# Kernel tuning notes

Hardware: AMD Instinct MI355X
Metric: run time of the kernel (lower is better)

The kernel has to match this reference:

```python
import jax, jax.numpy as jnp
import numpy as np
import math


def butterfly_mult_untied(twiddle, x, increasing_stride=True):
    """twiddle: (nstack, m, n//2, 2, 2); x: (batch, nstack, n)."""
    b, nstack, n = x.shape
    m = twiddle.shape[1]
    out = x
    for idx in range(m):  # loop over log2(n) stages (structural, not data dim)
        log_stride = idx if increasing_stride else m - 1 - idx
        stride = 1 << log_stride
        nb = n // (2 * stride)
        # (nstack, nb, stride, 2, 2) -> (nstack, nb, 2, 2, stride)
        t = jnp.transpose(twiddle[:, idx].reshape(nstack, nb, stride, 2, 2), (0, 1, 3, 4, 2))
        o = out.reshape(b, nstack, nb, 1, 2, stride)
        out = (t * o).sum(axis=4).reshape(b, nstack, n)
    return out


def setup_inputs() -> dict:
    key = jax.random.key(0)
    k1, k2, k3 = jax.random.split(key, 3)
    batch, in_size, out_size = 32768, 1024, 1024
    m = int(math.ceil(math.log2(in_size)))  # 10
    nstack = 1
    x = jax.random.normal(k1, (batch, in_size), dtype=jnp.float32)
    # 'regular' non-ortho init: randn / sqrt(2)
    twiddle = jax.random.normal(k2, (nstack, m, in_size // 2, 2, 2), dtype=jnp.float32) / math.sqrt(2)
    bound = 1 / math.sqrt(in_size)
    bias = jax.random.uniform(k3, (out_size,), dtype=jnp.float32, minval=-bound, maxval=bound)
    return {"x": x, "twiddle": twiddle, "bias": bias}


def reference(x, twiddle, bias):
    batch, in_size = x.shape
    nstack = twiddle.shape[0]
    out_size = bias.shape[0]
    # pre_process: in_size is a power of 2 and nstack==1 -> just stack
    out = jnp.broadcast_to(x[:, None, :], (batch, nstack, in_size))
    out = butterfly_mult_untied(twiddle, out, increasing_stride=True)
    # post_process: flatten nstack, slice to out_size, add bias
    out = out.reshape(batch, nstack * in_size)[:, :out_size] + bias
    return out
```

## Files before the change

kernel.cpp:

```cpp
#include <hip/hip_runtime.h>


constexpr int N = 1024;
constexpr int B_ROWS = 4;
constexpr int WAVES = 4;
constexpr int WBUF  = 1344;


template<int ST>
__device__ __forceinline__ void stageA(float (&v)[4][16],
                                       const float4* __restrict__ tw4,
                                       const int lane)
{
    constexpr int s = 1 << ST;
    #pragma unroll
    for (int pi = 0; pi < 8; ++pi) {
        const int jl = ((pi >> ST) << (ST + 1)) | (pi & (s - 1));
        const int jh = jl + s;
        const int e  = 16 * lane + jl;
        const int pr = ((e >> (ST + 1)) << ST) | (e & (s - 1));
        const float4 t = tw4[ST * 512 + pr];
        #pragma unroll
        for (int r = 0; r < 4; ++r) {
            const float lo = v[r][jl], hi = v[r][jh];
            v[r][jl] = t.x * lo + t.y * hi;
            v[r][jh] = t.z * lo + t.w * hi;
        }
    }
}

template<int ST>
__device__ __forceinline__ void stageE(float (&v)[4][16],
                                       const float4* __restrict__ tw4,
                                       const int lane)
{
    constexpr int s  = 1 << ST;
    constexpr int km = 1 << (ST - 4);
    const int a = lane >> 4, b = lane & 15;
    #pragma unroll
    for (int pi = 0; pi < 8; ++pi) {
        const int kl = ((pi >> (ST - 4)) << (ST - 3)) | (pi & (km - 1));
        const int kh = kl + km;
        const int e  = 256 * a + 16 * kl + b;
        const int pr = ((e >> (ST + 1)) << ST) | (e & (s - 1));
        const float4 t = tw4[ST * 512 + pr];
        #pragma unroll
        for (int r = 0; r < 4; ++r) {
            const float lo = v[r][kl], hi = v[r][kh];
            v[r][kl] = t.x * lo + t.y * hi;
            v[r][kh] = t.z * lo + t.w * hi;
        }
    }
}

template<int ST>
__device__ __forceinline__ void stageF(float (&v)[4][16],
                                       const float4* __restrict__ tw4,
                                       const int lane)
{
    constexpr int s  = 1 << ST;
    constexpr int am = 1 << (ST - 8);
    #pragma unroll
    for (int pi = 0; pi < 8; ++pi) {
        const int ai   = pi >> 2;
        const int b10  = pi & 3;
        const int a_lo = ((ai >> (ST - 8)) << (ST - 7)) | (ai & (am - 1));
        const int a_hi = a_lo + am;
        const int ml   = a_lo * 4 + b10;
        const int mh   = a_hi * 4 + b10;
        const int e    = a_lo * 256 + 4 * lane + b10;
        const int pr   = ((e >> (ST + 1)) << ST) | (e & (s - 1));
        const float4 t = tw4[ST * 512 + pr];
        #pragma unroll
        for (int r = 0; r < 4; ++r) {
            const float lo = v[r][ml], hi = v[r][mh];
            v[r][ml] = t.x * lo + t.y * hi;
            v[r][mh] = t.z * lo + t.w * hi;
        }
    }
}

__global__ __launch_bounds__(256, 2)
void butterfly_kernel(const float* __restrict__ x,
                      const float* __restrict__ tw,
                      const float* __restrict__ bias,
                      float* __restrict__ out)
{
    __shared__ __align__(16) float tl[WAVES][WBUF];

    const int t    = threadIdx.x;
    const int lane = t & 63;
    const int g    = t >> 6;
    float* wb = tl[g];

    const size_t row0 = ((size_t)blockIdx.x * WAVES + g) * B_ROWS;
    const float4* tw4 = (const float4*)tw;

    float v[4][16];

    #pragma unroll
    for (int r = 0; r < 4; ++r) {
        const float* px = x + (row0 + r) * N + 16 * lane;
        #pragma unroll
        for (int i = 0; i < 4; ++i) {
            const float4 d = *(const float4*)(px + 4 * i);
            v[r][4 * i + 0] = d.x; v[r][4 * i + 1] = d.y;
            v[r][4 * i + 2] = d.z; v[r][4 * i + 3] = d.w;
        }
    }

    stageA<0>(v, tw4, lane);
    stageA<1>(v, tw4, lane);
    stageA<2>(v, tw4, lane);
    stageA<3>(v, tw4, lane);

    {
        const int wbase = 20 * lane + 16 * ((lane >> 4) & 3);
        const int a = lane >> 4, b = lane & 15;
        const int rb = 336 * a + b;
        #pragma unroll
        for (int r = 0; r < 4; ++r) {
            #pragma unroll
            for (int i = 0; i < 4; ++i)
                *(float4*)(wb + wbase + 4 * i) =
                    make_float4(v[r][4 * i + 0], v[r][4 * i + 1],
                                v[r][4 * i + 2], v[r][4 * i + 3]);
            #pragma unroll
            for (int k = 0; k < 16; ++k)
                v[r][k] = wb[rb + 20 * k];
        }
    }

    stageE<4>(v, tw4, lane);
    stageE<5>(v, tw4, lane);
    stageE<6>(v, tw4, lane);
    stageE<7>(v, tw4, lane);

    {
        const int a = lane >> 4, b = lane & 15;
        const int wbase = 336 * a + 20 * b;
        const int rb = 80 * (lane & 3) + (lane >> 2);
        #pragma unroll
        for (int r = 0; r < 4; ++r) {
            #pragma unroll
            for (int i = 0; i < 4; ++i)
                *(float4*)(wb + wbase + 4 * i) =
                    make_float4(v[r][4 * i + 0], v[r][4 * i + 1],
                                v[r][4 * i + 2], v[r][4 * i + 3]);
            #pragma unroll
            for (int m = 0; m < 16; ++m)
                v[r][m] = wb[rb + 336 * (m >> 2) + 20 * (m & 3)];
        }
    }

    stageF<8>(v, tw4, lane);
    stageF<9>(v, tw4, lane);

    #pragma unroll
    for (int r = 0; r < 4; ++r) {
        float* po = out + (row0 + r) * N + 4 * lane;
        #pragma unroll
        for (int aa = 0; aa < 4; ++aa) {
            const float4 bb = *(const float4*)(bias + aa * 256 + 4 * lane);
            float4 o;
            o.x = v[r][4 * aa + 0] + bb.x;
            o.y = v[r][4 * aa + 1] + bb.y;
            o.z = v[r][4 * aa + 2] + bb.z;
            o.w = v[r][4 * aa + 3] + bb.w;
            *(float4*)(po + aa * 256) = o;
        }
    }
}

extern "C" void kernel_launch(void* const* d_in, const int* in_sizes, int n_in,
                              void* d_out, int out_size, void* d_ws, size_t ws_size,
                              hipStream_t stream) {
    const float* x    = (const float*)d_in[0];
    const float* tw   = (const float*)d_in[1];
    const float* bias = (const float*)d_in[2];
    float* out        = (float*)d_out;

    const int batch  = in_sizes[0] / N;
    const int blocks = batch / (B_ROWS * WAVES);
    hipLaunchKernelGGL(butterfly_kernel, dim3(blocks), dim3(256), 0, stream,
                       x, tw, bias, out);
}
```

Measured before the change: 261.5 us.

## Stage per-block twiddle tables in LDS in lane-contiguous order

Each block now gathers the twiddles for stages 0-3 and 8-9 from global memory into shared memory, permuted so each lane reads a contiguous float4 indexed by butterfly and lane. The aim is to replace scattered global twiddle reads per wave with conflict-free LDS reads. The stage-A table is reused as the transpose scratch after a barrier, and bias loads are hoisted out of the row loop. In exchange it adds a per-block prologue, two block barriers, and more LDS per block, which could limit occupancy.

```diff
diff --git a/kernel.cpp b/kernel.cpp
--- a/kernel.cpp
+++ b/kernel.cpp
@@ -9,7 +9,7 @@
 
 template<int ST>
 __device__ __forceinline__ void stageA(float (&v)[4][16],
-                                       const float4* __restrict__ tw4,
+                                       const float4* __restrict__ tbl,
                                        const int lane)
 {
     constexpr int s = 1 << ST;
@@ -17,9 +17,7 @@
     for (int pi = 0; pi < 8; ++pi) {
         const int jl = ((pi >> ST) << (ST + 1)) | (pi & (s - 1));
         const int jh = jl + s;
-        const int e  = 16 * lane + jl;
-        const int pr = ((e >> (ST + 1)) << ST) | (e & (s - 1));
-        const float4 t = tw4[ST * 512 + pr];
+        const float4 t = tbl[(pi << 6) | lane];
         #pragma unroll
         for (int r = 0; r < 4; ++r) {
             const float lo = v[r][jl], hi = v[r][jh];
@@ -55,10 +53,9 @@
 
 template<int ST>
 __device__ __forceinline__ void stageF(float (&v)[4][16],
-                                       const float4* __restrict__ tw4,
+                                       const float4* __restrict__ tbl,
                                        const int lane)
 {
-    constexpr int s  = 1 << ST;
     constexpr int am = 1 << (ST - 8);
     #pragma unroll
     for (int pi = 0; pi < 8; ++pi) {
@@ -68,9 +65,7 @@
         const int a_hi = a_lo + am;
         const int ml   = a_lo * 4 + b10;
         const int mh   = a_hi * 4 + b10;
-        const int e    = a_lo * 256 + 4 * lane + b10;
-        const int pr   = ((e >> (ST + 1)) << ST) | (e & (s - 1));
-        const float4 t = tw4[ST * 512 + pr];
+        const float4 t = tbl[(pi << 6) | lane];
         #pragma unroll
         for (int r = 0; r < 4; ++r) {
             const float lo = v[r][ml], hi = v[r][mh];
@@ -86,15 +81,47 @@
                       const float* __restrict__ bias,
                       float* __restrict__ out)
 {
-    __shared__ __align__(16) float tl[WAVES][WBUF];
+    __shared__ __align__(16) float4 tblA[4][512];
+    __shared__ __align__(16) float4 tblF[2][512];
 
     const int t    = threadIdx.x;
     const int lane = t & 63;
     const int g    = t >> 6;
-    float* wb = tl[g];
+
+    const float4* tw4 = (const float4*)tw;
+
+    #pragma unroll
+    for (int st = 0; st < 4; ++st) {
+        const int s = 1 << st;
+        #pragma unroll
+        for (int h = 0; h < 2; ++h) {
+            const int idx = t + 256 * h;
+            const int pi = idx >> 6, ln = idx & 63;
+            const int jl = ((pi >> st) << (st + 1)) | (pi & (s - 1));
+            const int e  = 16 * ln + jl;
+            const int pr = ((e >> (st + 1)) << st) | (e & (s - 1));
+            tblA[st][idx] = tw4[st * 512 + pr];
+        }
+    }
+    #pragma unroll
+    for (int f = 0; f < 2; ++f) {
+        const int st = 8 + f;
+        const int s  = 1 << st;
+        const int am = 1 << (st - 8);
+        #pragma unroll
+        for (int h = 0; h < 2; ++h) {
+            const int idx = t + 256 * h;
+            const int pi = idx >> 6, ln = idx & 63;
+            const int ai = pi >> 2, b10 = pi & 3;
+            const int a_lo = ((ai >> (st - 8)) << (st - 7)) | (ai & (am - 1));
+            const int e  = a_lo * 256 + 4 * ln + b10;
+            const int pr = ((e >> (st + 1)) << st) | (e & (s - 1));
+            tblF[f][idx] = tw4[st * 512 + pr];
+        }
+    }
+    __syncthreads();
 
     const size_t row0 = ((size_t)blockIdx.x * WAVES + g) * B_ROWS;
-    const float4* tw4 = (const float4*)tw;
 
     float v[4][16];
 
@@ -109,10 +136,13 @@
         }
     }
 
-    stageA<0>(v, tw4, lane);
-    stageA<1>(v, tw4, lane);
-    stageA<2>(v, tw4, lane);
-    stageA<3>(v, tw4, lane);
+    stageA<0>(v, tblA[0], lane);
+    stageA<1>(v, tblA[1], lane);
+    stageA<2>(v, tblA[2], lane);
+    stageA<3>(v, tblA[3], lane);
+
+    __syncthreads();
+    float* wb = reinterpret_cast<float*>(tblA) + g * WBUF;
 
     {
         const int wbase = 20 * lane + 16 * ((lane >> 4) & 3);
@@ -153,20 +183,23 @@
         }
     }
 
-    stageF<8>(v, tw4, lane);
-    stageF<9>(v, tw4, lane);
-
+    stageF<8>(v, tblF[0], lane);
+    stageF<9>(v, tblF[1], lane);
+
+    float4 bb[4];
+    #pragma unroll
+    for (int aa = 0; aa < 4; ++aa)
+        bb[aa] = *(const float4*)(bias + aa * 256 + 4 * lane);
     #pragma unroll
     for (int r = 0; r < 4; ++r) {
         float* po = out + (row0 + r) * N + 4 * lane;
         #pragma unroll
         for (int aa = 0; aa < 4; ++aa) {
-            const float4 bb = *(const float4*)(bias + aa * 256 + 4 * lane);
             float4 o;
-            o.x = v[r][4 * aa + 0] + bb.x;
-            o.y = v[r][4 * aa + 1] + bb.y;
-            o.z = v[r][4 * aa + 2] + bb.z;
-            o.w = v[r][4 * aa + 3] + bb.w;
+            o.x = v[r][4 * aa + 0] + bb[aa].x;
+            o.y = v[r][4 * aa + 1] + bb[aa].y;
+            o.z = v[r][4 * aa + 2] + bb[aa].z;
+            o.w = v[r][4 * aa + 3] + bb[aa].w;
             *(float4*)(po + aa * 256) = o;
         }
     }
```

After: 246.2 us. -5.8%, faster.
